# Performance work log

Measured on AMD Instinct MI355X. Metric: run time of the kernel, lower is better.

The kernel has to match this reference:

```python
import jax, jax.numpy as jnp
import numpy as np

AUX_COEF = 0.001
Z_COEF = 0.001


def setup_inputs() -> dict:
    key = jax.random.key(0)
    ks = jax.random.split(key, 6)
    B, S, H, E, F = 4, 2048, 1024, 8, 2048
    scale_h = 1.0 / np.sqrt(H)
    scale_f = 1.0 / np.sqrt(F)
    return {
        "hidden_states": jax.random.normal(ks[0], (B, S, H), jnp.float32),
        "router_w": jax.random.normal(ks[1], (E, H), jnp.float32) * scale_h,
        "w1": jax.random.normal(ks[2], (E, H, F), jnp.float32) * scale_h,
        "b1": jax.random.normal(ks[3], (E, F), jnp.float32) * 0.01,
        "w2": jax.random.normal(ks[4], (E, F, H), jnp.float32) * scale_f,
        "b2": jax.random.normal(ks[5], (E, H), jnp.float32) * 0.01,
        "num_experts_per_tok": 2,
    }


def reference(hidden_states, router_w, w1, b1, w2, b2, num_experts_per_tok):
    B, S, H = hidden_states.shape
    E = router_w.shape[0]
    x = hidden_states.reshape(-1, H)  # [T, H]

    # Router
    logits = jnp.einsum('th,eh->te', x, router_w)  # [T, E]
    logp = jax.nn.log_softmax(logits, axis=-1)
    probs = jnp.exp(logp)

    # Top-k routing mask (note: original code does NOT weight by top_k probs)
    _, top_idx = jax.lax.top_k(probs, num_experts_per_tok)  # [T, K]
    mask = jax.nn.one_hot(top_idx, E, dtype=x.dtype).sum(axis=-2)  # [T, E] 0/1

    # Losses: KL(probs || uniform) with torch kl_div(batchmean over dim0=B) + z-loss
    ideal = 1.0 / E
    aux_loss = (ideal * (jnp.log(jnp.float32(ideal)) - logp)).sum() / B * AUX_COEF
    z_loss = jnp.mean(jnp.square(logits)) * Z_COEF
    router_loss = aux_loss + z_loss

    # Dense grouped expert MLP, combined with 0/1 routing mask
    h = jnp.einsum('th,ehf->tef', x, w1) + b1  # [T, E, F]
    h = jax.nn.silu(h)
    y = jnp.einsum('tef,efh->teh', h, w2) + b2  # [T, E, H]
    out = jnp.einsum('teh,te->th', y, mask).reshape(B, S, H)
    return out, router_loss
```

## Files before the change

### kernel.cpp

```cpp
#include <hip/hip_runtime.h>
#include <stdint.h>

#define T_TOK 8192
#define H_DIM 1024
#define E_NUM 8
#define F_DIM 2048
#define BATCH 4
#define AUX_COEF 0.001f
#define Z_COEF 0.001f

#define NBLK_TOK 32

#define GBM 256
#define GBN 256
#define GBK 32
#define MT_CAP 16

typedef __bf16 bf16x8 __attribute__((ext_vector_type(8)));
typedef float f32x4 __attribute__((ext_vector_type(4)));

__device__ __forceinline__ unsigned short f2bf(float f) {
    union { float f; uint32_t u; } v; v.f = f;
    uint32_t u = v.u;
    return (unsigned short)((u + 0x7FFFu + ((u >> 16) & 1u)) >> 16);
}
__device__ __forceinline__ float bf2f(unsigned short u) {
    union { uint32_t u; float f; } v; v.u = ((uint32_t)u) << 16; return v.f;
}

__device__ __forceinline__ void gl_lds16(const void* g, void* l) {
    __builtin_amdgcn_global_load_lds((const __attribute__((address_space(1))) uint32_t*)g,
                                     (__attribute__((address_space(3))) uint32_t*)l, 16, 0, 0);
}

__global__ void transpose_conv_kernel(const float* __restrict__ in, unsigned short* __restrict__ out,
                                      int R, int C) {
    __shared__ float tile[32][33];
    int e = blockIdx.z;
    const float* ine = in + (size_t)e * R * C;
    unsigned short* oute = out + (size_t)e * R * C;
    int tx = threadIdx.x & 31, ty = threadIdx.x >> 5;
    int c0 = blockIdx.x * 32, r0 = blockIdx.y * 32;
#pragma unroll
    for (int i = 0; i < 4; i++) {
        int r = r0 + ty + i * 8;
        tile[ty + i * 8][tx] = ine[(size_t)r * C + c0 + tx];
    }
    __syncthreads();
#pragma unroll
    for (int i = 0; i < 4; i++) {
        int c = c0 + ty + i * 8;
        oute[(size_t)c * R + r0 + tx] = f2bf(tile[tx][ty + i * 8]);
    }
}

__global__ void router_kernel(const float* __restrict__ x, const float* __restrict__ rw,
                              unsigned short* __restrict__ xb,
                              int* __restrict__ top2, float2* __restrict__ loss_part) {
    int wave = threadIdx.x >> 6;
    int lane = threadIdx.x & 63;
    int t = blockIdx.x * 4 + wave;
    const float4* xr = (const float4*)(x + (size_t)t * H_DIM);
    float4 xv[4];
#pragma unroll
    for (int k = 0; k < 4; k++) xv[k] = xr[lane + 64 * k];
    uint2* xo = (uint2*)(xb + (size_t)t * H_DIM);
#pragma unroll
    for (int k = 0; k < 4; k++) {
        uint2 o;
        o.x = (uint32_t)f2bf(xv[k].x) | ((uint32_t)f2bf(xv[k].y) << 16);
        o.y = (uint32_t)f2bf(xv[k].z) | ((uint32_t)f2bf(xv[k].w) << 16);
        xo[lane + 64 * k] = o;
    }
    float acc[E_NUM];
#pragma unroll
    for (int e = 0; e < E_NUM; e++) {
        const float4* rr = (const float4*)(rw + e * H_DIM);
        float s = 0.f;
#pragma unroll
        for (int k = 0; k < 4; k++) {
            float4 r = rr[lane + 64 * k];
            s += xv[k].x * r.x + xv[k].y * r.y + xv[k].z * r.z + xv[k].w * r.w;
        }
        acc[e] = s;
    }
#pragma unroll
    for (int e = 0; e < E_NUM; e++) {
        float v = acc[e];
#pragma unroll
        for (int off = 32; off; off >>= 1) v += __shfl_xor(v, off);
        acc[e] = v;
    }
    __shared__ float red[8];
    if (lane == 0) {
        float mx = acc[0];
#pragma unroll
        for (int e = 1; e < E_NUM; e++) mx = fmaxf(mx, acc[e]);
        float s = 0.f;
#pragma unroll
        for (int e = 0; e < E_NUM; e++) s += expf(acc[e] - mx);
        float lse = mx + logf(s);
        float slogp = 0.f, ssq = 0.f;
#pragma unroll
        for (int e = 0; e < E_NUM; e++) { slogp += acc[e] - lse; ssq += acc[e] * acc[e]; }
        int i1 = 0; float m1 = acc[0];
#pragma unroll
        for (int e = 1; e < E_NUM; e++) if (acc[e] > m1) { m1 = acc[e]; i1 = e; }
        int i2 = -1; float m2 = -1e30f;
#pragma unroll
        for (int e = 0; e < E_NUM; e++) if (e != i1 && acc[e] > m2) { m2 = acc[e]; i2 = e; }
        top2[t] = i1 | (i2 << 8);
        red[wave] = slogp;
        red[4 + wave] = ssq;
    }
    __syncthreads();
    if (threadIdx.x == 0) {
        float2 p;
        p.x = red[0] + red[1] + red[2] + red[3];
        p.y = red[4] + red[5] + red[6] + red[7];
        loss_part[blockIdx.x] = p;
    }
}

__global__ void hist_kernel(const int* __restrict__ top2, int* __restrict__ blockcounts) {
    __shared__ int cnt[E_NUM];
    if (threadIdx.x < E_NUM) cnt[threadIdx.x] = 0;
    __syncthreads();
    int t = blockIdx.x * 256 + threadIdx.x;
    int v = top2[t];
    atomicAdd(&cnt[v & 255], 1);
    atomicAdd(&cnt[v >> 8], 1);
    __syncthreads();
    if (threadIdx.x < E_NUM) blockcounts[blockIdx.x * E_NUM + threadIdx.x] = cnt[threadIdx.x];
}

__global__ void scan_kernel(const int* __restrict__ blockcounts, const float2* __restrict__ loss_part,
                            int* __restrict__ counts, int* __restrict__ basep, int* __restrict__ offs,
                            float* __restrict__ loss_out) {
    __shared__ float redx[4], redy[4];
    int tid = threadIdx.x;
    float sx = 0.f, sy = 0.f;
    for (int i = tid; i < T_TOK / 4; i += 256) {
        float2 p = loss_part[i];
        sx += p.x; sy += p.y;
    }
#pragma unroll
    for (int off = 32; off; off >>= 1) { sx += __shfl_xor(sx, off); sy += __shfl_xor(sy, off); }
    if ((tid & 63) == 0) { redx[tid >> 6] = sx; redy[tid >> 6] = sy; }
    __syncthreads();
    if (tid == 0) {
        float slogp = redx[0] + redx[1] + redx[2] + redx[3];
        float ssq = redy[0] + redy[1] + redy[2] + redy[3];
        float ideal = 1.0f / E_NUM;
        float aux = ideal * ((float)T_TOK * E_NUM * logf(ideal) - slogp) / BATCH * AUX_COEF;
        float z = ssq / ((float)T_TOK * E_NUM) * Z_COEF;
        loss_out[0] = aux + z;
    }
    if (tid < E_NUM) {
        int s = 0;
        for (int b = 0; b < NBLK_TOK; b++) s += blockcounts[b * E_NUM + tid];
        counts[tid] = s;
    }
    __syncthreads();
    if (tid == 0) {
        int s = 0;
        for (int e = 0; e < E_NUM; e++) { basep[e] = s; s += counts[e]; }
    }
    __syncthreads();
    if (tid < E_NUM) {
        int o = basep[tid];
        for (int b = 0; b < NBLK_TOK; b++) { offs[b * E_NUM + tid] = o; o += blockcounts[b * E_NUM + tid]; }
    }
}

__global__ void scatter_kernel(const int* __restrict__ top2, const int* __restrict__ offs,
                               int* __restrict__ rowlist, int* __restrict__ posv) {
    __shared__ int cur[E_NUM];
    if (threadIdx.x < E_NUM) cur[threadIdx.x] = 0;
    __syncthreads();
    int t = blockIdx.x * 256 + threadIdx.x;
    int v = top2[t];
    int e0 = v & 255, e1 = v >> 8;
    int r0 = atomicAdd(&cur[e0], 1);
    int r1 = atomicAdd(&cur[e1], 1);
    int p0 = offs[blockIdx.x * E_NUM + e0] + r0;
    int p1 = offs[blockIdx.x * E_NUM + e1] + r1;
    rowlist[p0] = t;
    rowlist[p1] = t;
    posv[t] = p0 | (p1 << 16);
}

__global__ void combine_kernel(const int* __restrict__ top2, const int* __restrict__ posv,
                               const unsigned short* __restrict__ ybuf, const float* __restrict__ b2,
                               float* __restrict__ out) {
    int t = blockIdx.x;
    int v = top2[t];
    int p = posv[t];
    int e0 = v & 255, e1 = v >> 8;
    int p0 = p & 0xffff, p1 = (p >> 16) & 0xffff;
    int i = threadIdx.x;
    const ushort4* y0 = (const ushort4*)(ybuf + (size_t)p0 * H_DIM);
    const ushort4* y1 = (const ushort4*)(ybuf + (size_t)p1 * H_DIM);
    const float4* q0 = (const float4*)(b2 + (size_t)e0 * H_DIM);
    const float4* q1 = (const float4*)(b2 + (size_t)e1 * H_DIM);
    ushort4 a = y0[i], b = y1[i];
    float4 c0 = q0[i], c1 = q1[i];
    float4 o;
    o.x = bf2f(a.x) + bf2f(b.x) + c0.x + c1.x;
    o.y = bf2f(a.y) + bf2f(b.y) + c0.y + c1.y;
    o.z = bf2f(a.z) + bf2f(b.z) + c0.z + c1.z;
    o.w = bf2f(a.w) + bf2f(b.w) + c0.w + c1.w;
    ((float4*)(out + (size_t)t * H_DIM))[i] = o;
}

template<int KD, int NTILES_N, bool IS_G1>
__global__ __launch_bounds__(512, 2)
void gemm_big(const unsigned short* __restrict__ A,
              const unsigned short* __restrict__ Bt,
              const float* __restrict__ bias_p,
              const int* __restrict__ rowlist,
              const int* __restrict__ basep,
              const int* __restrict__ counts,
              unsigned short* __restrict__ Out)
{
    constexpr int ND = NTILES_N * GBN;
    constexpr int NKT = KD / GBK;
    static_assert(NKT >= 4, "ring needs >=4 K-tiles");

    int bid = blockIdx.x;
    int e = bid & 7;
    int q = bid >> 3;
    int nt = q % NTILES_N;
    int mt = q / NTILES_N;
    int n_e = counts[e];
    if (mt * GBM >= n_e) return;
    int base_e = basep[e];

    __shared__ __attribute__((aligned(16))) unsigned char lds[4 * 32768];

    int tid = threadIdx.x;
    int wv = tid >> 6, lane = tid & 63;

    int srow = tid >> 2;
    int schunk = tid & 3;
    const unsigned short* aS[2];
    const unsigned short* bS[2];
#pragma unroll
    for (int c = 0; c < 2; c++) {
        int r = c * 128 + srow;
        if (IS_G1) {
            int ra = min(mt * GBM + r, n_e - 1);
            int tok = rowlist[base_e + ra];
            aS[c] = A + (size_t)tok * KD + schunk * 8;
        } else {
            int ra = base_e + min(mt * GBM + r, n_e - 1);
            aS[c] = A + (size_t)ra * KD + schunk * 8;
        }
        bS[c] = Bt + ((size_t)e * ND + nt * GBN + r) * KD + schunk * 8;
    }
    char* ldsw = (char*)lds + wv * 1024;

    int mlane = lane & 15, quad = lane >> 4;
    int wr = (wv >> 2) * 128;
    int wc = (wv & 3) * 64;
    int aOff[8], bOff[4];
#pragma unroll
    for (int mi = 0; mi < 8; mi++) aOff[mi] = (wr + mi * 16 + mlane) * 64 + quad * 16;
#pragma unroll
    for (int ni = 0; ni < 4; ni++) bOff[ni] = 16384 + (wc + ni * 16 + mlane) * 64 + quad * 16;

    f32x4 acc[8][4] = {};

    auto stage = [&](int t) {
        char* sb = ldsw + (size_t)(t & 3) * 32768;
        const unsigned short* a0 = aS[0] + t * GBK;
        const unsigned short* a1 = aS[1] + t * GBK;
        const unsigned short* b0 = bS[0] + t * GBK;
        const unsigned short* b1 = bS[1] + t * GBK;
        gl_lds16(a0, sb);
        gl_lds16(a1, sb + 8192);
        gl_lds16(b0, sb + 16384);
        gl_lds16(b1, sb + 24576);
    };
    auto compute = [&](int t) {
        char* sb = (char*)lds + (size_t)(t & 3) * 32768;
        __builtin_amdgcn_s_setprio(1);
        bf16x8 bfr[4];
#pragma unroll
        for (int ni = 0; ni < 4; ni++) bfr[ni] = *(const bf16x8*)(sb + bOff[ni]);
#pragma unroll
        for (int mi = 0; mi < 8; mi++) {
            bf16x8 af = *(const bf16x8*)(sb + aOff[mi]);
#pragma unroll
            for (int ni = 0; ni < 4; ni++)
                acc[mi][ni] = __builtin_amdgcn_mfma_f32_16x16x32_bf16(af, bfr[ni], acc[mi][ni], 0, 0, 0);
        }
        __builtin_amdgcn_s_setprio(0);
    };

    stage(0); stage(1); stage(2);

    for (int kt = 0; kt < NKT - 3; ++kt) {
        asm volatile("s_waitcnt vmcnt(8) lgkmcnt(0)" ::: "memory");
        __builtin_amdgcn_s_barrier();
        __builtin_amdgcn_sched_barrier(0);
        stage(kt + 3);
        compute(kt);
    }
    asm volatile("s_waitcnt vmcnt(8) lgkmcnt(0)" ::: "memory");
    __builtin_amdgcn_s_barrier();
    __builtin_amdgcn_sched_barrier(0);
    compute(NKT - 3);
    asm volatile("s_waitcnt vmcnt(4) lgkmcnt(0)" ::: "memory");
    __builtin_amdgcn_s_barrier();
    __builtin_amdgcn_sched_barrier(0);
    compute(NKT - 2);
    asm volatile("s_waitcnt vmcnt(0) lgkmcnt(0)" ::: "memory");
    __builtin_amdgcn_s_barrier();
    __builtin_amdgcn_sched_barrier(0);
    compute(NKT - 1);

    float bias[4];
#pragma unroll
    for (int ni = 0; ni < 4; ni++) {
        if (IS_G1) bias[ni] = bias_p[(size_t)e * ND + nt * GBN + wc + ni * 16 + mlane];
        else bias[ni] = 0.f;
    }
#pragma unroll
    for (int mi = 0; mi < 8; mi++) {
        int mbase = mt * GBM + wr + mi * 16 + quad * 4;
#pragma unroll
        for (int r = 0; r < 4; r++) {
            int m = mbase + r;
            if (m < n_e) {
                unsigned short* orow = Out + (size_t)(base_e + m) * ND + nt * GBN + wc + mlane;
#pragma unroll
                for (int ni = 0; ni < 4; ni++) {
                    float c = acc[mi][ni][r] + bias[ni];
                    if (IS_G1) c = c / (1.f + __expf(-c));
                    orow[ni * 16] = f2bf(c);
                }
            }
        }
    }
}

extern "C" void kernel_launch(void* const* d_in, const int* in_sizes, int n_in,
                              void* d_out, int out_size, void* d_ws, size_t ws_size,
                              hipStream_t stream) {
    const float* x = (const float*)d_in[0];
    const float* rw = (const float*)d_in[1];
    const float* w1 = (const float*)d_in[2];
    const float* b1 = (const float*)d_in[3];
    const float* w2 = (const float*)d_in[4];
    const float* b2 = (const float*)d_in[5];
    float* out = (float*)d_out;

    char* ws = (char*)d_ws;
    int* counts      = (int*)(ws + 0);
    int* basep       = (int*)(ws + 64);
    int* blockcounts = (int*)(ws + 128);
    int* offs        = (int*)(ws + 2048);
    float2* loss_part = (float2*)(ws + 4096);
    int* top2        = (int*)(ws + 32768);
    int* rowlist     = (int*)(ws + 65536);
    int* posv        = (int*)(ws + 131072);
    unsigned short* xb  = (unsigned short*)(ws + 163840);
    unsigned short* w1t = (unsigned short*)(ws + 163840 + 16777216ULL);
    unsigned short* w2t = (unsigned short*)(ws + 163840 + 16777216ULL + 33554432ULL);
    unsigned short* h1  = (unsigned short*)(ws + 163840 + 16777216ULL + 2ULL * 33554432ULL);
    unsigned short* ybuf = w1t;

    transpose_conv_kernel<<<dim3(64, 32, 8), 256, 0, stream>>>(w1, w1t, H_DIM, F_DIM);
    transpose_conv_kernel<<<dim3(32, 64, 8), 256, 0, stream>>>(w2, w2t, F_DIM, H_DIM);
    router_kernel<<<T_TOK / 4, 256, 0, stream>>>(x, rw, xb, top2, loss_part);
    hist_kernel<<<NBLK_TOK, 256, 0, stream>>>(top2, blockcounts);
    scan_kernel<<<1, 256, 0, stream>>>(blockcounts, loss_part, counts, basep, offs,
                                       out + (size_t)T_TOK * H_DIM);
    scatter_kernel<<<NBLK_TOK, 256, 0, stream>>>(top2, offs, rowlist, posv);
    gemm_big<H_DIM, F_DIM / GBN, true><<<8 * MT_CAP * (F_DIM / GBN), 512, 0, stream>>>(
        xb, w1t, b1, rowlist, basep, counts, h1);
    gemm_big<F_DIM, H_DIM / GBN, false><<<8 * MT_CAP * (H_DIM / GBN), 512, 0, stream>>>(
        h1, w2t, nullptr, rowlist, basep, counts, ybuf);
    combine_kernel<<<T_TOK, 256, 0, stream>>>(top2, posv, ybuf, b2, out);
}
```

Baseline: 453.6 us.

## Restructure expert GEMM into double-buffered quadrant-phased pipeline with swizzled LDS

Replaces the 4-deep K-tile ring (K=32) with a double-buffered K=64 pipeline where each K step is split into four MFMA quadrant phases, interleaving half-tile global->LDS loads between them. LDS rows are XOR-swizzled to reduce bank conflicts on the wider 128-byte rows. Aims to overlap memory and MFMA work more finely and halve per-K loop overhead, at the cost of many more barriers per iteration and higher register use for held fragments.

```diff
diff --git a/kernel.cpp b/kernel.cpp
--- a/kernel.cpp
+++ b/kernel.cpp
@@ -13,7 +13,7 @@
 
 #define GBM 256
 #define GBN 256
-#define GBK 32
+#define GBK 64
 #define MT_CAP 16
 
 typedef __bf16 bf16x8 __attribute__((ext_vector_type(8)));
@@ -215,17 +215,17 @@
 
 template<int KD, int NTILES_N, bool IS_G1>
 __global__ __launch_bounds__(512, 2)
-void gemm_big(const unsigned short* __restrict__ A,
-              const unsigned short* __restrict__ Bt,
-              const float* __restrict__ bias_p,
-              const int* __restrict__ rowlist,
-              const int* __restrict__ basep,
-              const int* __restrict__ counts,
-              unsigned short* __restrict__ Out)
+void gemm8p(const unsigned short* __restrict__ A,
+            const unsigned short* __restrict__ Bt,
+            const float* __restrict__ bias_p,
+            const int* __restrict__ rowlist,
+            const int* __restrict__ basep,
+            const int* __restrict__ counts,
+            unsigned short* __restrict__ Out)
 {
     constexpr int ND = NTILES_N * GBN;
     constexpr int NKT = KD / GBK;
-    static_assert(NKT >= 4, "ring needs >=4 K-tiles");
+    static_assert(NKT >= 4, "pipeline needs >=4 K-tiles");
 
     int bid = blockIdx.x;
     int e = bid & 7;
@@ -236,89 +236,144 @@
     if (mt * GBM >= n_e) return;
     int base_e = basep[e];
 
-    __shared__ __attribute__((aligned(16))) unsigned char lds[4 * 32768];
+    __shared__ __attribute__((aligned(16))) unsigned char lds[2][65536];
 
     int tid = threadIdx.x;
     int wv = tid >> 6, lane = tid & 63;
 
-    int srow = tid >> 2;
-    int schunk = tid & 3;
-    const unsigned short* aS[2];
-    const unsigned short* bS[2];
-#pragma unroll
-    for (int c = 0; c < 2; c++) {
-        int r = c * 128 + srow;
+    int srow = tid >> 3;
+    int gc = (tid & 7) ^ (srow & 7);
+    const unsigned short* aS[4];
+    const unsigned short* bS[4];
+#pragma unroll
+    for (int i = 0; i < 4; i++) {
+        int r = srow + i * 64;
+        size_t ra;
         if (IS_G1) {
-            int ra = min(mt * GBM + r, n_e - 1);
-            int tok = rowlist[base_e + ra];
-            aS[c] = A + (size_t)tok * KD + schunk * 8;
+            int rr = min(mt * GBM + r, n_e - 1);
+            ra = (size_t)rowlist[base_e + rr];
         } else {
-            int ra = base_e + min(mt * GBM + r, n_e - 1);
-            aS[c] = A + (size_t)ra * KD + schunk * 8;
-        }
-        bS[c] = Bt + ((size_t)e * ND + nt * GBN + r) * KD + schunk * 8;
-    }
-    char* ldsw = (char*)lds + wv * 1024;
+            ra = (size_t)(base_e + min(mt * GBM + r, n_e - 1));
+        }
+        aS[i] = A + ra * KD + gc * 8;
+        bS[i] = Bt + ((size_t)e * ND + nt * GBN + r) * KD + gc * 8;
+    }
+
+    auto stageA = [&](int buf, int h, int t) {
+        char* d = (char*)lds + buf * 65536 + h * 16384 + wv * 1024;
+        gl_lds16(aS[h * 2 + 0] + t * GBK, d);
+        gl_lds16(aS[h * 2 + 1] + t * GBK, d + 8192);
+    };
+    auto stageB = [&](int buf, int h, int t) {
+        char* d = (char*)lds + buf * 65536 + 32768 + h * 16384 + wv * 1024;
+        gl_lds16(bS[h * 2 + 0] + t * GBK, d);
+        gl_lds16(bS[h * 2 + 1] + t * GBK, d + 8192);
+    };
 
     int mlane = lane & 15, quad = lane >> 4;
     int wr = (wv >> 2) * 128;
     int wc = (wv & 3) * 64;
-    int aOff[8], bOff[4];
-#pragma unroll
-    for (int mi = 0; mi < 8; mi++) aOff[mi] = (wr + mi * 16 + mlane) * 64 + quad * 16;
-#pragma unroll
-    for (int ni = 0; ni < 4; ni++) bOff[ni] = 16384 + (wc + ni * 16 + mlane) * 64 + quad * 16;
+    int xk0 = (quad * 16) ^ ((mlane & 7) << 4);
+    int xk1 = (64 + quad * 16) ^ ((mlane & 7) << 4);
+    int aRow = (wr + mlane) * 128;
+    int bRow = 32768 + (wc + mlane) * 128;
 
     f32x4 acc[8][4] = {};
-
-    auto stage = [&](int t) {
-        char* sb = ldsw + (size_t)(t & 3) * 32768;
-        const unsigned short* a0 = aS[0] + t * GBK;
-        const unsigned short* a1 = aS[1] + t * GBK;
-        const unsigned short* b0 = bS[0] + t * GBK;
-        const unsigned short* b1 = bS[1] + t * GBK;
-        gl_lds16(a0, sb);
-        gl_lds16(a1, sb + 8192);
-        gl_lds16(b0, sb + 16384);
-        gl_lds16(b1, sb + 24576);
-    };
-    auto compute = [&](int t) {
-        char* sb = (char*)lds + (size_t)(t & 3) * 32768;
+    bf16x8 a03[4][2], a47[4][2], b01[2][2], b23[2][2];
+
+    stageA(0, 0, 0); stageA(0, 1, 0); stageB(0, 0, 0); stageB(0, 1, 0);
+    if (NKT > 1) { stageB(1, 0, 1); stageA(1, 0, 1); }
+    asm volatile("s_waitcnt vmcnt(4)" ::: "memory");
+    __builtin_amdgcn_s_barrier();
+
+    for (int t = 0; t < NKT; ++t) {
+        const char* Ab = (const char*)lds + (t & 1) * 65536;
+        int nb = (t + 1) & 1;
+
+#pragma unroll
+        for (int mi = 0; mi < 4; mi++) {
+            a03[mi][0] = *(const bf16x8*)(Ab + aRow + mi * 2048 + xk0);
+            a03[mi][1] = *(const bf16x8*)(Ab + aRow + mi * 2048 + xk1);
+        }
+#pragma unroll
+        for (int ni = 0; ni < 2; ni++) {
+            b01[ni][0] = *(const bf16x8*)(Ab + bRow + ni * 2048 + xk0);
+            b01[ni][1] = *(const bf16x8*)(Ab + bRow + ni * 2048 + xk1);
+        }
+        if (t + 1 < NKT) stageB(nb, 1, t + 1);
+        __builtin_amdgcn_s_barrier();
+        asm volatile("s_waitcnt lgkmcnt(0)" ::: "memory");
+        __builtin_amdgcn_sched_barrier(0);
         __builtin_amdgcn_s_setprio(1);
-        bf16x8 bfr[4];
-#pragma unroll
-        for (int ni = 0; ni < 4; ni++) bfr[ni] = *(const bf16x8*)(sb + bOff[ni]);
-#pragma unroll
-        for (int mi = 0; mi < 8; mi++) {
-            bf16x8 af = *(const bf16x8*)(sb + aOff[mi]);
-#pragma unroll
-            for (int ni = 0; ni < 4; ni++)
-                acc[mi][ni] = __builtin_amdgcn_mfma_f32_16x16x32_bf16(af, bfr[ni], acc[mi][ni], 0, 0, 0);
-        }
+#pragma unroll
+        for (int ks = 0; ks < 2; ks++)
+#pragma unroll
+            for (int mi = 0; mi < 4; mi++)
+#pragma unroll
+                for (int ni = 0; ni < 2; ni++)
+                    acc[mi][ni] = __builtin_amdgcn_mfma_f32_16x16x32_bf16(a03[mi][ks], b01[ni][ks], acc[mi][ni], 0, 0, 0);
         __builtin_amdgcn_s_setprio(0);
-    };
-
-    stage(0); stage(1); stage(2);
-
-    for (int kt = 0; kt < NKT - 3; ++kt) {
-        asm volatile("s_waitcnt vmcnt(8) lgkmcnt(0)" ::: "memory");
-        __builtin_amdgcn_s_barrier();
+        __builtin_amdgcn_s_barrier();
+
+#pragma unroll
+        for (int ni = 0; ni < 2; ni++) {
+            b23[ni][0] = *(const bf16x8*)(Ab + bRow + (ni + 2) * 2048 + xk0);
+            b23[ni][1] = *(const bf16x8*)(Ab + bRow + (ni + 2) * 2048 + xk1);
+        }
+        if (t + 1 < NKT) stageA(nb, 1, t + 1);
+        __builtin_amdgcn_s_barrier();
+        asm volatile("s_waitcnt lgkmcnt(0)" ::: "memory");
         __builtin_amdgcn_sched_barrier(0);
-        stage(kt + 3);
-        compute(kt);
-    }
-    asm volatile("s_waitcnt vmcnt(8) lgkmcnt(0)" ::: "memory");
-    __builtin_amdgcn_s_barrier();
-    __builtin_amdgcn_sched_barrier(0);
-    compute(NKT - 3);
-    asm volatile("s_waitcnt vmcnt(4) lgkmcnt(0)" ::: "memory");
-    __builtin_amdgcn_s_barrier();
-    __builtin_amdgcn_sched_barrier(0);
-    compute(NKT - 2);
-    asm volatile("s_waitcnt vmcnt(0) lgkmcnt(0)" ::: "memory");
-    __builtin_amdgcn_s_barrier();
-    __builtin_amdgcn_sched_barrier(0);
-    compute(NKT - 1);
+        __builtin_amdgcn_s_setprio(1);
+#pragma unroll
+        for (int ks = 0; ks < 2; ks++)
+#pragma unroll
+            for (int mi = 0; mi < 4; mi++)
+#pragma unroll
+                for (int ni = 0; ni < 2; ni++)
+                    acc[mi][ni + 2] = __builtin_amdgcn_mfma_f32_16x16x32_bf16(a03[mi][ks], b23[ni][ks], acc[mi][ni + 2], 0, 0, 0);
+        __builtin_amdgcn_s_setprio(0);
+        __builtin_amdgcn_s_barrier();
+
+#pragma unroll
+        for (int mi = 0; mi < 4; mi++) {
+            a47[mi][0] = *(const bf16x8*)(Ab + aRow + (mi + 4) * 2048 + xk0);
+            a47[mi][1] = *(const bf16x8*)(Ab + aRow + (mi + 4) * 2048 + xk1);
+        }
+        if (t + 2 < NKT) stageB(t & 1, 0, t + 2);
+        __builtin_amdgcn_s_barrier();
+        asm volatile("s_waitcnt lgkmcnt(0)" ::: "memory");
+        __builtin_amdgcn_sched_barrier(0);
+        __builtin_amdgcn_s_setprio(1);
+#pragma unroll
+        for (int ks = 0; ks < 2; ks++)
+#pragma unroll
+            for (int mi = 0; mi < 4; mi++)
+#pragma unroll
+                for (int ni = 0; ni < 2; ni++)
+                    acc[mi + 4][ni] = __builtin_amdgcn_mfma_f32_16x16x32_bf16(a47[mi][ks], b01[ni][ks], acc[mi + 4][ni], 0, 0, 0);
+        __builtin_amdgcn_s_setprio(0);
+        __builtin_amdgcn_s_barrier();
+
+        if (t + 2 < NKT) stageA(t & 1, 0, t + 2);
+        __builtin_amdgcn_s_barrier();
+        __builtin_amdgcn_sched_barrier(0);
+        __builtin_amdgcn_s_setprio(1);
+#pragma unroll
+        for (int ks = 0; ks < 2; ks++)
+#pragma unroll
+            for (int mi = 0; mi < 4; mi++)
+#pragma unroll
+                for (int ni = 0; ni < 2; ni++)
+                    acc[mi + 4][ni + 2] = __builtin_amdgcn_mfma_f32_16x16x32_bf16(a47[mi][ks], b23[ni][ks], acc[mi + 4][ni + 2], 0, 0, 0);
+        __builtin_amdgcn_s_setprio(0);
+        if (t + 2 < NKT) {
+            asm volatile("s_waitcnt vmcnt(4)" ::: "memory");
+        } else {
+            asm volatile("s_waitcnt vmcnt(0)" ::: "memory");
+        }
+        __builtin_amdgcn_s_barrier();
+    }
 
     float bias[4];
 #pragma unroll
@@ -378,9 +433,9 @@
     scan_kernel<<<1, 256, 0, stream>>>(blockcounts, loss_part, counts, basep, offs,
                                        out + (size_t)T_TOK * H_DIM);
     scatter_kernel<<<NBLK_TOK, 256, 0, stream>>>(top2, offs, rowlist, posv);
-    gemm_big<H_DIM, F_DIM / GBN, true><<<8 * MT_CAP * (F_DIM / GBN), 512, 0, stream>>>(
+    gemm8p<H_DIM, F_DIM / GBN, true><<<8 * MT_CAP * (F_DIM / GBN), 512, 0, stream>>>(
         xb, w1t, b1, rowlist, basep, counts, h1);
-    gemm_big<F_DIM, H_DIM / GBN, false><<<8 * MT_CAP * (H_DIM / GBN), 512, 0, stream>>>(
+    gemm8p<F_DIM, H_DIM / GBN, false><<<8 * MT_CAP * (H_DIM / GBN), 512, 0, stream>>>(
         h1, w2t, nullptr, rowlist, basep, counts, ybuf);
     combine_kernel<<<T_TOK, 256, 0, stream>>>(top2, posv, ybuf, b2, out);
 }
```

Measured after the change: 449.5 us. No clear change (-0.9%).
